# Optimization experiments

Measured on AMD Instinct MI355X. Metric: run time of the kernel, lower is better.

The kernel has to match this reference:

```python
import jax, jax.numpy as jnp
import numpy as np

IN_SIZE = 8192
N_PART = 64
EMBED = IN_SIZE // N_PART  # 128
BATCH = 8192
LN_EPS = 1e-5
ATT_EPS = 1e-7


def setup_inputs() -> dict:
    key = jax.random.key(0)
    ks = jax.random.split(key, 9)
    s = 1.0 / np.sqrt(EMBED)
    return {
        "x": jax.random.normal(ks[0], (BATCH, IN_SIZE), dtype=jnp.float32),
        "Wq": jax.random.uniform(ks[1], (EMBED, EMBED), jnp.float32, -s, s),
        "bq": jax.random.uniform(ks[2], (EMBED,), jnp.float32, -s, s),
        "Wk": jax.random.uniform(ks[3], (EMBED, EMBED), jnp.float32, -s, s),
        "bk": jax.random.uniform(ks[4], (EMBED,), jnp.float32, -s, s),
        "Wv": jax.random.uniform(ks[5], (EMBED, EMBED), jnp.float32, -s, s),
        "bv": jax.random.uniform(ks[6], (EMBED,), jnp.float32, -s, s),
        "ln_w": jnp.ones((IN_SIZE,), jnp.float32),
        "ln_b": jnp.zeros((IN_SIZE,), jnp.float32),
    }


def reference(x, Wq, bq, Wk, bk, Wv, bv, ln_w, ln_b):
    B = x.shape[0]
    # LayerNorm over in_size
    mu = jnp.mean(x, axis=-1, keepdims=True)
    var = jnp.mean((x - mu) ** 2, axis=-1, keepdims=True)
    x_norm = (x - mu) * jax.lax.rsqrt(var + LN_EPS) * ln_w + ln_b
    _x = x_norm.reshape(B, N_PART, EMBED)  # [b, l, d]
    # elu(lin(x)) + 1 feature maps (torch Linear: x @ W.T + b)
    Q = jax.nn.elu(jnp.einsum("bld,ed->ble", _x, Wq) + bq) + 1.0
    K = jax.nn.elu(jnp.einsum("bld,ed->ble", _x, Wk) + bk) + 1.0
    V = jnp.einsum("bld,ed->ble", _x, Wv) + bv
    # KV[b,k,j] = sum_i K[b,i,j] V[b,i,k]
    KV = jnp.einsum("bij,bik->bkj", K, V)
    Ksum = jnp.sum(K, axis=1)  # [b, d]
    norm = 1.0 / (jnp.einsum("bld,bd->bl", Q, Ksum) + ATT_EPS)
    prod = jnp.einsum("bld,bmd,bl->blm", Q, KV, norm)  # [b, l, v_dim]
    return prod.reshape(B, -1) + x
```

## Files before the change

kernel.cpp:

```cpp
#include <hip/hip_runtime.h>

typedef __attribute__((ext_vector_type(8))) __bf16 bf16x8;
typedef __attribute__((ext_vector_type(8))) unsigned short ushort8v;
typedef __attribute__((ext_vector_type(4))) float f32x4;

__device__ __forceinline__ unsigned short f2bf(float f) {
  return __builtin_bit_cast(unsigned short, (__bf16)f);
}

__device__ __forceinline__ int qoff(int row, int colb) {
  return row * 256 + (colb ^ ((row & 7) << 4));
}
__device__ __forceinline__ int toff(int row, int colb) {
  return row * 128 + (colb ^ ((row & 7) << 4));
}

__device__ __forceinline__ void bar_lds() {
  asm volatile("s_waitcnt lgkmcnt(0)" ::: "memory");
  __builtin_amdgcn_s_barrier();
}

__global__ void prep_w(const float* __restrict__ Wq, const float* __restrict__ Wk,
                       const float* __restrict__ Wv, unsigned short* __restrict__ ws) {
  int i = blockIdx.x * 256 + threadIdx.x;
  if (i >= 3 * 16384) return;
  const float* s = (i < 16384) ? Wq : (i < 32768 ? Wk : Wv);
  ws[i] = f2bf(s[i & 16383]);
}

__global__ __launch_bounds__(512, 2) void fused_attn(
    const float* __restrict__ x, const unsigned short* __restrict__ wsW,
    const float* __restrict__ bq, const float* __restrict__ bk, const float* __restrict__ bv,
    const float* __restrict__ ln_w, const float* __restrict__ ln_b,
    float* __restrict__ out) {
  __shared__ __align__(16) unsigned char smem[74368];
  unsigned char* sA  = smem;
  unsigned char* sQ  = smem + 16384;
  unsigned char* sK  = smem + 32768;
  unsigned char* sVT = smem + 49152;
  unsigned char* sS  = smem + 65536;
  float* redS  = (float*)(smem + 73728);
  float* pPart = (float*)(smem + 73856);

  const int tid = threadIdx.x;
  const int lane = tid & 63;
  const int w = tid >> 6;
  const int l15 = lane & 15;
  const int l4 = lane >> 4;
  const size_t base = (size_t)blockIdx.x * (8 * 8192);

  bf16x8 wf[3][4];
  const int col = (w << 4) + l15;
#pragma unroll
  for (int m = 0; m < 3; ++m) {
    const unsigned short* wp = wsW + m * 16384 + col * 128 + (l4 << 3);
#pragma unroll
    for (int kk = 0; kk < 4; ++kk)
      wf[m][kk] = *(const bf16x8*)(wp + kk * 32);
  }
  const float biasQ = bq[col], biasK = bk[col], biasV = bv[col];

  const int row_x = tid >> 3;
  const int c0 = (tid & 7) << 4;
  float lw[16], lb[16];
  {
    const float* pw = ln_w + row_x * 128 + c0;
    const float* pb = ln_b + row_x * 128 + c0;
#pragma unroll
    for (int i = 0; i < 4; ++i) {
      float4 a = *(const float4*)(pw + i * 4);
      lw[i*4+0]=a.x; lw[i*4+1]=a.y; lw[i*4+2]=a.z; lw[i*4+3]=a.w;
      float4 b = *(const float4*)(pb + i * 4);
      lb[i*4+0]=b.x; lb[i*4+1]=b.y; lb[i*4+2]=b.z; lb[i*4+3]=b.w;
    }
  }

  float xv[16];
  {
    const float* xp = x + base + (size_t)row_x * 128 + c0;
#pragma unroll
    for (int i = 0; i < 4; ++i) {
      float4 a = *(const float4*)(xp + i * 4);
      xv[i*4+0]=a.x; xv[i*4+1]=a.y; xv[i*4+2]=a.z; xv[i*4+3]=a.w;
    }
  }
  {
    float s1 = 0.f, s2 = 0.f;
#pragma unroll
    for (int i = 0; i < 16; ++i) { s1 += xv[i]; s2 += xv[i] * xv[i]; }
#pragma unroll
    for (int off = 32; off > 0; off >>= 1) {
      s1 += __shfl_xor(s1, off, 64);
      s2 += __shfl_xor(s2, off, 64);
    }
    if (lane == 0) { redS[w] = s1; redS[8 + w] = s2; }
  }
  bar_lds();

#pragma unroll 1
  for (int r = 0; r < 8; ++r) {
    const size_t bofs = base + (size_t)r * 8192;

    const float* rb = redS + (r & 1) * 16;
    float t1 = 0.f, t2 = 0.f;
#pragma unroll
    for (int p = 0; p < 8; ++p) { t1 += rb[p]; t2 += rb[8 + p]; }
    const float mu = t1 * (1.f / 8192.f);
    const float rstd = rsqrtf(t2 * (1.f / 8192.f) - mu * mu + 1e-5f);
#pragma unroll
    for (int h = 0; h < 2; ++h) {
      ushort8v t;
#pragma unroll
      for (int j = 0; j < 8; ++j)
        t[j] = f2bf((xv[h*8+j] - mu) * rstd * lw[h*8+j] + lb[h*8+j]);
      *(ushort8v*)(sA + qoff(row_x, (c0 << 1) + h * 16)) = t;
    }
    if (r < 7) {
      const float* xp = x + bofs + 8192 + (size_t)row_x * 128 + c0;
#pragma unroll
      for (int i = 0; i < 4; ++i) {
        float4 a = *(const float4*)(xp + i * 4);
        xv[i*4+0]=a.x; xv[i*4+1]=a.y; xv[i*4+2]=a.z; xv[i*4+3]=a.w;
      }
    }
    bar_lds();

#pragma unroll
    for (int mt = 0; mt < 4; ++mt) {
      bf16x8 aq[4];
#pragma unroll
      for (int kk = 0; kk < 4; ++kk)
        aq[kk] = *(const bf16x8*)(sA + qoff(mt * 16 + l15, kk * 64 + (l4 << 4)));
      const int i0m = mt * 16 + (l4 << 2);
      f32x4 aQ = {0,0,0,0}, aK = {0,0,0,0}, aV = {0,0,0,0};
#pragma unroll
      for (int kk = 0; kk < 4; ++kk) {
        aQ = __builtin_amdgcn_mfma_f32_16x16x32_bf16(aq[kk], wf[0][kk], aQ, 0, 0, 0);
        aK = __builtin_amdgcn_mfma_f32_16x16x32_bf16(aq[kk], wf[1][kk], aK, 0, 0, 0);
        aV = __builtin_amdgcn_mfma_f32_16x16x32_bf16(aq[kk], wf[2][kk], aV, 0, 0, 0);
      }
#pragma unroll
      for (int rr = 0; rr < 4; ++rr) {
        float zq = aQ[rr] + biasQ; zq = zq > 0.f ? zq + 1.f : __expf(zq);
        *(unsigned short*)(sQ + qoff(i0m + rr, col * 2)) = f2bf(zq);
        float zk = aK[rr] + biasK; zk = zk > 0.f ? zk + 1.f : __expf(zk);
        *(unsigned short*)(sK + qoff(i0m + rr, col * 2)) = f2bf(zk);
      }
      ushort4 pk;
      pk.x = f2bf(aV[0] + biasV); pk.y = f2bf(aV[1] + biasV);
      pk.z = f2bf(aV[2] + biasV); pk.w = f2bf(aV[3] + biasV);
      *(ushort4*)(sVT + toff(col, i0m * 2)) = pk;
    }
    bar_lds();

    const int rt = w >> 1;
    const int h = w & 1;
    const int i0s = rt * 16 + (l4 << 2);
    f32x4 xr[4];
    {
      bf16x8 aq[4];
#pragma unroll
      for (int kk = 0; kk < 4; ++kk)
        aq[kk] = *(const bf16x8*)(sQ + qoff(rt * 16 + l15, kk * 64 + (l4 << 4)));
#pragma unroll
      for (int nt = 0; nt < 4; ++nt) {
        const int l = nt * 16 + l15;
        const int mb = (w << 4) + (l4 << 2);
        xr[nt] = *(const f32x4*)(x + bofs + (size_t)l * 128 + mb);
      }
      f32x4 accS[2];
#pragma unroll
      for (int nt = 0; nt < 2; ++nt) {
        const int ntg = h * 2 + nt;
        f32x4 acc = {0,0,0,0};
#pragma unroll
        for (int kk = 0; kk < 4; ++kk) {
          bf16x8 bk_ = *(const bf16x8*)(sK + qoff(ntg * 16 + l15, kk * 64 + (l4 << 4)));
          acc = __builtin_amdgcn_mfma_f32_16x16x32_bf16(aq[kk], bk_, acc, 0, 0, 0);
        }
        accS[nt] = acc;
      }
      float p[4];
#pragma unroll
      for (int rr = 0; rr < 4; ++rr) p[rr] = accS[0][rr] + accS[1][rr];
#pragma unroll
      for (int off = 1; off < 16; off <<= 1) {
#pragma unroll
        for (int rr = 0; rr < 4; ++rr) p[rr] += __shfl_xor(p[rr], off, 64);
      }
      if (l15 == 0) {
#pragma unroll
        for (int rr = 0; rr < 4; ++rr)
          pPart[w * 16 + (l4 << 2) + rr] = p[rr];
      }
      if (r < 7) {
        float n1 = 0.f, n2 = 0.f;
#pragma unroll
        for (int i = 0; i < 16; ++i) { n1 += xv[i]; n2 += xv[i] * xv[i]; }
#pragma unroll
        for (int off = 32; off > 0; off >>= 1) {
          n1 += __shfl_xor(n1, off, 64);
          n2 += __shfl_xor(n2, off, 64);
        }
        if (lane == 0) {
          float* nb = redS + ((r + 1) & 1) * 16;
          nb[w] = n1; nb[8 + w] = n2;
        }
      }
#pragma unroll
      for (int nt = 0; nt < 2; ++nt) {
        const int ntg = h * 2 + nt;
#pragma unroll
        for (int rr = 0; rr < 4; ++rr)
          *(unsigned short*)(sS + toff(i0s + rr, (ntg * 16 + l15) * 2)) = f2bf(accS[nt][rr]);
      }
    }
    bar_lds();

    {
      float nv[4];
#pragma unroll
      for (int nt = 0; nt < 4; ++nt)
        nv[nt] = 1.f / (pPart[nt * 32 + l15] + pPart[nt * 32 + 16 + l15] + 1e-7f);
      bf16x8 av[2];
#pragma unroll
      for (int kk = 0; kk < 2; ++kk)
        av[kk] = *(const bf16x8*)(sVT + toff((w << 4) + l15, kk * 64 + (l4 << 4)));
#pragma unroll
      for (int nt = 0; nt < 4; ++nt) {
        bf16x8 bs0 = *(const bf16x8*)(sS + toff(nt * 16 + l15, (l4 << 4)));
        bf16x8 bs1 = *(const bf16x8*)(sS + toff(nt * 16 + l15, 64 + (l4 << 4)));
        f32x4 acc = {0,0,0,0};
        acc = __builtin_amdgcn_mfma_f32_16x16x32_bf16(av[0], bs0, acc, 0, 0, 0);
        acc = __builtin_amdgcn_mfma_f32_16x16x32_bf16(av[1], bs1, acc, 0, 0, 0);
        const int l = nt * 16 + l15;
        const int mb = (w << 4) + (l4 << 2);
        const size_t idx = bofs + (size_t)l * 128 + mb;
        f32x4 o;
        o[0] = acc[0] * nv[nt] + xr[nt][0];
        o[1] = acc[1] * nv[nt] + xr[nt][1];
        o[2] = acc[2] * nv[nt] + xr[nt][2];
        o[3] = acc[3] * nv[nt] + xr[nt][3];
        *(f32x4*)(out + idx) = o;
      }
    }
  }
}

extern "C" void kernel_launch(void* const* d_in, const int* in_sizes, int n_in,
                              void* d_out, int out_size, void* d_ws, size_t ws_size,
                              hipStream_t stream) {
  const float* x   = (const float*)d_in[0];
  const float* Wq  = (const float*)d_in[1];
  const float* bq  = (const float*)d_in[2];
  const float* Wk  = (const float*)d_in[3];
  const float* bk  = (const float*)d_in[4];
  const float* Wv  = (const float*)d_in[5];
  const float* bv  = (const float*)d_in[6];
  const float* lnw = (const float*)d_in[7];
  const float* lnb = (const float*)d_in[8];
  unsigned short* ws = (unsigned short*)d_ws;
  float* out = (float*)d_out;

  prep_w<<<192, 256, 0, stream>>>(Wq, Wk, Wv, ws);
  fused_attn<<<1024, 512, 0, stream>>>(x, ws, bq, bk, bv, lnw, lnb, out);
}
```

Baseline: 198.7 us.

## Software-pipeline fused attention stages across rows with double-buffered LDS

Restructures the per-block row loop into a skewed software pipeline. Each iteration does QKV projection and scores for row r, the output GEMM and residual store for row r-1, and LayerNorm staging for row r+1. All LDS buffers (A, Q, K, VT, S, partial sums) are double-buffered, which cuts barriers per row from four to two. LDS grows to about 145 KB, so launch bounds drop to one 512-thread block per CU, giving up occupancy in exchange for more overlap within a block.

```diff
diff --git a/kernel.cpp b/kernel.cpp
--- a/kernel.cpp
+++ b/kernel.cpp
@@ -28,19 +28,14 @@
   ws[i] = f2bf(s[i & 16383]);
 }
 
-__global__ __launch_bounds__(512, 2) void fused_attn(
+__global__ __launch_bounds__(512, 1) void fused_attn(
     const float* __restrict__ x, const unsigned short* __restrict__ wsW,
     const float* __restrict__ bq, const float* __restrict__ bk, const float* __restrict__ bv,
     const float* __restrict__ ln_w, const float* __restrict__ ln_b,
     float* __restrict__ out) {
-  __shared__ __align__(16) unsigned char smem[74368];
-  unsigned char* sA  = smem;
-  unsigned char* sQ  = smem + 16384;
-  unsigned char* sK  = smem + 32768;
-  unsigned char* sVT = smem + 49152;
-  unsigned char* sS  = smem + 65536;
-  float* redS  = (float*)(smem + 73728);
-  float* pPart = (float*)(smem + 73856);
+  __shared__ __align__(16) unsigned char smem[148608];
+  float* redS  = (float*)(smem + 147456);
+  float* pPart = (float*)(smem + 147584);
 
   const int tid = threadIdx.x;
   const int lane = tid & 63;
@@ -75,19 +70,19 @@
     }
   }
 
-  float xv[16];
+  float xvC[16], xvN[16];
   {
     const float* xp = x + base + (size_t)row_x * 128 + c0;
 #pragma unroll
     for (int i = 0; i < 4; ++i) {
       float4 a = *(const float4*)(xp + i * 4);
-      xv[i*4+0]=a.x; xv[i*4+1]=a.y; xv[i*4+2]=a.z; xv[i*4+3]=a.w;
+      xvC[i*4+0]=a.x; xvC[i*4+1]=a.y; xvC[i*4+2]=a.z; xvC[i*4+3]=a.w;
     }
   }
   {
     float s1 = 0.f, s2 = 0.f;
 #pragma unroll
-    for (int i = 0; i < 16; ++i) { s1 += xv[i]; s2 += xv[i] * xv[i]; }
+    for (int i = 0; i < 16; ++i) { s1 += xvC[i]; s2 += xvC[i] * xvC[i]; }
 #pragma unroll
     for (int off = 32; off > 0; off >>= 1) {
       s1 += __shfl_xor(s1, off, 64);
@@ -96,41 +91,74 @@
     if (lane == 0) { redS[w] = s1; redS[8 + w] = s2; }
   }
   bar_lds();
+  {
+    float t1 = 0.f, t2 = 0.f;
+#pragma unroll
+    for (int p = 0; p < 8; ++p) { t1 += redS[p]; t2 += redS[8 + p]; }
+    const float mu = t1 * (1.f / 8192.f);
+    const float rstd = rsqrtf(t2 * (1.f / 8192.f) - mu * mu + 1e-5f);
+    unsigned char* sA0 = smem;
+#pragma unroll
+    for (int h = 0; h < 2; ++h) {
+      ushort8v t;
+#pragma unroll
+      for (int j = 0; j < 8; ++j)
+        t[j] = f2bf((xvC[h*8+j] - mu) * rstd * lw[h*8+j] + lb[h*8+j]);
+      *(ushort8v*)(sA0 + qoff(row_x, (c0 << 1) + h * 16)) = t;
+    }
+    const float* xp = x + base + 8192 + (size_t)row_x * 128 + c0;
+#pragma unroll
+    for (int i = 0; i < 4; ++i) {
+      float4 a = *(const float4*)(xp + i * 4);
+      xvN[i*4+0]=a.x; xvN[i*4+1]=a.y; xvN[i*4+2]=a.z; xvN[i*4+3]=a.w;
+    }
+    float s1 = 0.f, s2 = 0.f;
+#pragma unroll
+    for (int i = 0; i < 16; ++i) { s1 += xvN[i]; s2 += xvN[i] * xvN[i]; }
+#pragma unroll
+    for (int off = 32; off > 0; off >>= 1) {
+      s1 += __shfl_xor(s1, off, 64);
+      s2 += __shfl_xor(s2, off, 64);
+    }
+    if (lane == 0) { redS[16 + w] = s1; redS[24 + w] = s2; }
+  }
+  bar_lds();
+#pragma unroll
+  for (int i = 0; i < 16; ++i) xvC[i] = xvN[i];
 
 #pragma unroll 1
   for (int r = 0; r < 8; ++r) {
+    const int cur = r & 1, nxt = cur ^ 1;
+    unsigned char* sAc  = smem + cur * 16384;
+    unsigned char* sAn  = smem + nxt * 16384;
+    unsigned char* sQc  = smem + 32768 + cur * 16384;
+    unsigned char* sKc  = smem + 65536 + cur * 16384;
+    unsigned char* sVTc = smem + 98304 + cur * 16384;
+    unsigned char* sVTn = smem + 98304 + nxt * 16384;
+    unsigned char* sSc  = smem + 131072 + cur * 8192;
+    unsigned char* sSn  = smem + 131072 + nxt * 8192;
+    float* redC = redS + cur * 16;
+    float* redN = redS + nxt * 16;
+    float* pPc = pPart + cur * 128;
+    float* pPn = pPart + nxt * 128;
     const size_t bofs = base + (size_t)r * 8192;
 
-    const float* rb = redS + (r & 1) * 16;
-    float t1 = 0.f, t2 = 0.f;
-#pragma unroll
-    for (int p = 0; p < 8; ++p) { t1 += rb[p]; t2 += rb[8 + p]; }
-    const float mu = t1 * (1.f / 8192.f);
-    const float rstd = rsqrtf(t2 * (1.f / 8192.f) - mu * mu + 1e-5f);
-#pragma unroll
-    for (int h = 0; h < 2; ++h) {
-      ushort8v t;
-#pragma unroll
-      for (int j = 0; j < 8; ++j)
-        t[j] = f2bf((xv[h*8+j] - mu) * rstd * lw[h*8+j] + lb[h*8+j]);
-      *(ushort8v*)(sA + qoff(row_x, (c0 << 1) + h * 16)) = t;
-    }
-    if (r < 7) {
-      const float* xp = x + bofs + 8192 + (size_t)row_x * 128 + c0;
-#pragma unroll
-      for (int i = 0; i < 4; ++i) {
-        float4 a = *(const float4*)(xp + i * 4);
-        xv[i*4+0]=a.x; xv[i*4+1]=a.y; xv[i*4+2]=a.z; xv[i*4+3]=a.w;
-      }
-    }
-    bar_lds();
-
+    f32x4 xrP[4];
+    if (r >= 1) {
+      const size_t bofsP = bofs - 8192;
+#pragma unroll
+      for (int nt = 0; nt < 4; ++nt) {
+        const int l = nt * 16 + l15;
+        const int mb = (w << 4) + (l4 << 2);
+        xrP[nt] = *(const f32x4*)(x + bofsP + (size_t)l * 128 + mb);
+      }
+    }
 #pragma unroll
     for (int mt = 0; mt < 4; ++mt) {
       bf16x8 aq[4];
 #pragma unroll
       for (int kk = 0; kk < 4; ++kk)
-        aq[kk] = *(const bf16x8*)(sA + qoff(mt * 16 + l15, kk * 64 + (l4 << 4)));
+        aq[kk] = *(const bf16x8*)(sAc + qoff(mt * 16 + l15, kk * 64 + (l4 << 4)));
       const int i0m = mt * 16 + (l4 << 2);
       f32x4 aQ = {0,0,0,0}, aK = {0,0,0,0}, aV = {0,0,0,0};
 #pragma unroll
@@ -142,40 +170,56 @@
 #pragma unroll
       for (int rr = 0; rr < 4; ++rr) {
         float zq = aQ[rr] + biasQ; zq = zq > 0.f ? zq + 1.f : __expf(zq);
-        *(unsigned short*)(sQ + qoff(i0m + rr, col * 2)) = f2bf(zq);
+        *(unsigned short*)(sQc + qoff(i0m + rr, col * 2)) = f2bf(zq);
         float zk = aK[rr] + biasK; zk = zk > 0.f ? zk + 1.f : __expf(zk);
-        *(unsigned short*)(sK + qoff(i0m + rr, col * 2)) = f2bf(zk);
+        *(unsigned short*)(sKc + qoff(i0m + rr, col * 2)) = f2bf(zk);
       }
       ushort4 pk;
       pk.x = f2bf(aV[0] + biasV); pk.y = f2bf(aV[1] + biasV);
       pk.z = f2bf(aV[2] + biasV); pk.w = f2bf(aV[3] + biasV);
-      *(ushort4*)(sVT + toff(col, i0m * 2)) = pk;
+      *(ushort4*)(sVTc + toff(col, i0m * 2)) = pk;
+    }
+    if (r < 7) {
+      float t1 = 0.f, t2 = 0.f;
+#pragma unroll
+      for (int p = 0; p < 8; ++p) { t1 += redN[p]; t2 += redN[8 + p]; }
+      const float mu = t1 * (1.f / 8192.f);
+      const float rstd = rsqrtf(t2 * (1.f / 8192.f) - mu * mu + 1e-5f);
+#pragma unroll
+      for (int h = 0; h < 2; ++h) {
+        ushort8v t;
+#pragma unroll
+        for (int j = 0; j < 8; ++j)
+          t[j] = f2bf((xvC[h*8+j] - mu) * rstd * lw[h*8+j] + lb[h*8+j]);
+        *(ushort8v*)(sAn + qoff(row_x, (c0 << 1) + h * 16)) = t;
+      }
+      if (r < 6) {
+        const float* xp = x + bofs + 2 * 8192 + (size_t)row_x * 128 + c0;
+#pragma unroll
+        for (int i = 0; i < 4; ++i) {
+          float4 a = *(const float4*)(xp + i * 4);
+          xvN[i*4+0]=a.x; xvN[i*4+1]=a.y; xvN[i*4+2]=a.z; xvN[i*4+3]=a.w;
+        }
+      }
     }
     bar_lds();
 
     const int rt = w >> 1;
-    const int h = w & 1;
+    const int h2 = w & 1;
     const int i0s = rt * 16 + (l4 << 2);
-    f32x4 xr[4];
     {
       bf16x8 aq[4];
 #pragma unroll
       for (int kk = 0; kk < 4; ++kk)
-        aq[kk] = *(const bf16x8*)(sQ + qoff(rt * 16 + l15, kk * 64 + (l4 << 4)));
-#pragma unroll
-      for (int nt = 0; nt < 4; ++nt) {
-        const int l = nt * 16 + l15;
-        const int mb = (w << 4) + (l4 << 2);
-        xr[nt] = *(const f32x4*)(x + bofs + (size_t)l * 128 + mb);
-      }
+        aq[kk] = *(const bf16x8*)(sQc + qoff(rt * 16 + l15, kk * 64 + (l4 << 4)));
       f32x4 accS[2];
 #pragma unroll
       for (int nt = 0; nt < 2; ++nt) {
-        const int ntg = h * 2 + nt;
+        const int ntg = h2 * 2 + nt;
         f32x4 acc = {0,0,0,0};
 #pragma unroll
         for (int kk = 0; kk < 4; ++kk) {
-          bf16x8 bk_ = *(const bf16x8*)(sK + qoff(ntg * 16 + l15, kk * 64 + (l4 << 4)));
+          bf16x8 bk_ = *(const bf16x8*)(sKc + qoff(ntg * 16 + l15, kk * 64 + (l4 << 4)));
           acc = __builtin_amdgcn_mfma_f32_16x16x32_bf16(aq[kk], bk_, acc, 0, 0, 0);
         }
         accS[nt] = acc;
@@ -191,58 +235,99 @@
       if (l15 == 0) {
 #pragma unroll
         for (int rr = 0; rr < 4; ++rr)
-          pPart[w * 16 + (l4 << 2) + rr] = p[rr];
-      }
-      if (r < 7) {
-        float n1 = 0.f, n2 = 0.f;
-#pragma unroll
-        for (int i = 0; i < 16; ++i) { n1 += xv[i]; n2 += xv[i] * xv[i]; }
-#pragma unroll
-        for (int off = 32; off > 0; off >>= 1) {
-          n1 += __shfl_xor(n1, off, 64);
-          n2 += __shfl_xor(n2, off, 64);
-        }
-        if (lane == 0) {
-          float* nb = redS + ((r + 1) & 1) * 16;
-          nb[w] = n1; nb[8 + w] = n2;
-        }
+          pPc[w * 16 + (l4 << 2) + rr] = p[rr];
       }
 #pragma unroll
       for (int nt = 0; nt < 2; ++nt) {
-        const int ntg = h * 2 + nt;
+        const int ntg = h2 * 2 + nt;
 #pragma unroll
         for (int rr = 0; rr < 4; ++rr)
-          *(unsigned short*)(sS + toff(i0s + rr, (ntg * 16 + l15) * 2)) = f2bf(accS[nt][rr]);
-      }
-    }
-    bar_lds();
-
-    {
+          *(unsigned short*)(sSc + toff(i0s + rr, (ntg * 16 + l15) * 2)) = f2bf(accS[nt][rr]);
+      }
+    }
+    if (r < 6) {
+      float n1 = 0.f, n2 = 0.f;
+#pragma unroll
+      for (int i = 0; i < 16; ++i) { n1 += xvN[i]; n2 += xvN[i] * xvN[i]; }
+#pragma unroll
+      for (int off = 32; off > 0; off >>= 1) {
+        n1 += __shfl_xor(n1, off, 64);
+        n2 += __shfl_xor(n2, off, 64);
+      }
+      if (lane == 0) { redC[w] = n1; redC[8 + w] = n2; }
+    }
+    if (r >= 1) {
+      const size_t bofsP = bofs - 8192;
       float nv[4];
 #pragma unroll
       for (int nt = 0; nt < 4; ++nt)
-        nv[nt] = 1.f / (pPart[nt * 32 + l15] + pPart[nt * 32 + 16 + l15] + 1e-7f);
+        nv[nt] = 1.f / (pPn[nt * 32 + l15] + pPn[nt * 32 + 16 + l15] + 1e-7f);
       bf16x8 av[2];
 #pragma unroll
       for (int kk = 0; kk < 2; ++kk)
-        av[kk] = *(const bf16x8*)(sVT + toff((w << 4) + l15, kk * 64 + (l4 << 4)));
+        av[kk] = *(const bf16x8*)(sVTn + toff((w << 4) + l15, kk * 64 + (l4 << 4)));
 #pragma unroll
       for (int nt = 0; nt < 4; ++nt) {
-        bf16x8 bs0 = *(const bf16x8*)(sS + toff(nt * 16 + l15, (l4 << 4)));
-        bf16x8 bs1 = *(const bf16x8*)(sS + toff(nt * 16 + l15, 64 + (l4 << 4)));
+        bf16x8 bs0 = *(const bf16x8*)(sSn + toff(nt * 16 + l15, (l4 << 4)));
+        bf16x8 bs1 = *(const bf16x8*)(sSn + toff(nt * 16 + l15, 64 + (l4 << 4)));
         f32x4 acc = {0,0,0,0};
         acc = __builtin_amdgcn_mfma_f32_16x16x32_bf16(av[0], bs0, acc, 0, 0, 0);
         acc = __builtin_amdgcn_mfma_f32_16x16x32_bf16(av[1], bs1, acc, 0, 0, 0);
         const int l = nt * 16 + l15;
         const int mb = (w << 4) + (l4 << 2);
-        const size_t idx = bofs + (size_t)l * 128 + mb;
+        const size_t idx = bofsP + (size_t)l * 128 + mb;
         f32x4 o;
-        o[0] = acc[0] * nv[nt] + xr[nt][0];
-        o[1] = acc[1] * nv[nt] + xr[nt][1];
-        o[2] = acc[2] * nv[nt] + xr[nt][2];
-        o[3] = acc[3] * nv[nt] + xr[nt][3];
+        o[0] = acc[0] * nv[nt] + xrP[nt][0];
+        o[1] = acc[1] * nv[nt] + xrP[nt][1];
+        o[2] = acc[2] * nv[nt] + xrP[nt][2];
+        o[3] = acc[3] * nv[nt] + xrP[nt][3];
         *(f32x4*)(out + idx) = o;
       }
+    }
+    bar_lds();
+
+    if (r < 6) {
+#pragma unroll
+      for (int i = 0; i < 16; ++i) xvC[i] = xvN[i];
+    }
+  }
+
+  {
+    const size_t bofsP = base + 7 * 8192;
+    unsigned char* sVT1 = smem + 98304 + 16384;
+    unsigned char* sS1  = smem + 131072 + 8192;
+    float* pP1 = pPart + 128;
+    f32x4 xr7[4];
+#pragma unroll
+    for (int nt = 0; nt < 4; ++nt) {
+      const int l = nt * 16 + l15;
+      const int mb = (w << 4) + (l4 << 2);
+      xr7[nt] = *(const f32x4*)(x + bofsP + (size_t)l * 128 + mb);
+    }
+    float nv[4];
+#pragma unroll
+    for (int nt = 0; nt < 4; ++nt)
+      nv[nt] = 1.f / (pP1[nt * 32 + l15] + pP1[nt * 32 + 16 + l15] + 1e-7f);
+    bf16x8 av[2];
+#pragma unroll
+    for (int kk = 0; kk < 2; ++kk)
+      av[kk] = *(const bf16x8*)(sVT1 + toff((w << 4) + l15, kk * 64 + (l4 << 4)));
+#pragma unroll
+    for (int nt = 0; nt < 4; ++nt) {
+      bf16x8 bs0 = *(const bf16x8*)(sS1 + toff(nt * 16 + l15, (l4 << 4)));
+      bf16x8 bs1 = *(const bf16x8*)(sS1 + toff(nt * 16 + l15, 64 + (l4 << 4)));
+      f32x4 acc = {0,0,0,0};
+      acc = __builtin_amdgcn_mfma_f32_16x16x32_bf16(av[0], bs0, acc, 0, 0, 0);
+      acc = __builtin_amdgcn_mfma_f32_16x16x32_bf16(av[1], bs1, acc, 0, 0, 0);
+      const int l = nt * 16 + l15;
+      const int mb = (w << 4) + (l4 << 2);
+      const size_t idx = bofsP + (size_t)l * 128 + mb;
+      f32x4 o;
+      o[0] = acc[0] * nv[nt] + xr7[nt][0];
+      o[1] = acc[1] * nv[nt] + xr7[nt][1];
+      o[2] = acc[2] * nv[nt] + xr7[nt][2];
+      o[3] = acc[3] * nv[nt] + xr7[nt][3];
+      *(f32x4*)(out + idx) = o;
     }
   }
 }
```

New measurement: 189.8 us. 1.05x faster.
